# Kernel optimization log

Measured on AMD Instinct MI355X. Metric: run time of the kernel, lower is better.

## Reference

```python
import jax, jax.numpy as jnp
import numpy as np

B, C, D = 2, 2048, 1024   # batch, seq_len, hidden_size
I = 2048                  # intermediate_size (GLU hidden)
E, K = 8, 2               # n_experts, top_k
CF = 1.25                 # capacity factor


def setup_inputs() -> dict:
    key = jax.random.key(0)
    k1, k2, k3, k4 = jax.random.split(key, 4)
    scale = 0.02
    return {
        "hidden_states": jax.random.normal(k1, (B, C, D), jnp.float32),
        "Wg": jax.random.normal(k2, (E, D), jnp.float32) * scale,      # router gate weight [E, d]
        "W1": jax.random.normal(k3, (E, D, 2 * I), jnp.float32) * scale,  # expert in-proj
        "W2": jax.random.normal(k4, (E, I, D), jnp.float32) * scale,      # expert out-proj
    }


def reference(hidden_states, Wg, W1, W2):
    Bx, Cx, d = hidden_states.shape
    N = Bx * Cx
    cap = int(N * K * CF / E)  # exp_capacity (static)
    x = hidden_states.reshape(N, d)

    # --- router (eval mode: no noise) ---
    logits = x @ Wg.T                          # [N, E]
    top_v, top_i = jax.lax.top_k(logits, K)    # [N, K]
    gates = jax.nn.softmax(top_v, axis=-1)     # [N, K]

    # --- greedy capacity-limited assignment (token-major, then k), vectorized ---
    flat_e = top_i.reshape(N * K)              # expert id per (token, k) slot, in loop order
    gates_f = gates.reshape(N * K)
    tok = jnp.repeat(jnp.arange(N), K)         # token id per slot
    onehot = jax.nn.one_hot(flat_e, E, dtype=jnp.int32)
    pos = jnp.cumsum(onehot, axis=0) - 1       # running count per expert
    pos_f = jnp.take_along_axis(pos, flat_e[:, None], axis=1)[:, 0]
    keep = pos_f < cap                         # slots beyond capacity are dropped
    pos_safe = jnp.where(keep, pos_f, cap)     # out-of-range -> dropped by mode='drop'

    # --- dispatch: exp_batches[e, pos] = x[token] ---
    exp_batches = jnp.zeros((E, cap, d), x.dtype).at[flat_e, pos_safe].set(x[tok], mode='drop')

    # --- per-expert GLU MLP (batched over experts) ---
    h = jnp.einsum('ecd,edf->ecf', exp_batches, W1)       # [E, cap, 2I]
    inp, gate = jnp.split(h, 2, axis=-1)
    h = jax.nn.gelu(inp, approximate=False) * gate        # exact gelu, matches torch
    exp_out = jnp.einsum('eci,eid->ecd', h, W2)           # [E, cap, d]

    # --- combine: equals exp_mask.view(N,-1) @ exp_out.view(-1,d) ---
    gathered = exp_out[flat_e, jnp.minimum(pos_safe, cap - 1)]  # [N*K, d]
    contrib = jnp.where(keep, gates_f, 0.0)[:, None] * gathered
    out = jax.ops.segment_sum(contrib, tok, num_segments=N)    # [N, d]
    return out.reshape(Bx, Cx, d)
```

## Files before the change

### kernel.cpp

```cpp
#include <hip/hip_runtime.h>
#include <hip/hip_bf16.h>
#include <math.h>

#define N_TOK 4096
#define DIM   1024
#define NEXP  8
#define IDIM  2048
#define TWOI  4096
#define CAP   1280

#define W1_BLOCKS (64 * 16 * NEXP)
#define W2_BLOCKS (16 * 32 * NEXP)
#define ROUTER_BLOCKS (N_TOK / 4)

#define G1X 32
#define G1Y 10
#define G1_TRANS_Z ((W2_BLOCKS + G1X * G1Y - 1) / (G1X * G1Y))

using short8  = __attribute__((ext_vector_type(8))) short;
using floatx4 = __attribute__((ext_vector_type(4))) float;

__device__ __forceinline__ unsigned short f2b(float f) {
  __hip_bfloat16 h = __float2bfloat16(f);
  return *reinterpret_cast<unsigned short*>(&h);
}

__device__ __forceinline__ void async16(const unsigned short* g, unsigned short* l) {
  __builtin_amdgcn_global_load_lds(
      (const __attribute__((address_space(1))) unsigned int*)g,
      (__attribute__((address_space(3))) unsigned int*)l,
      16, 0, 0);
}

__global__ __launch_bounds__(256) void prologue_kernel(const float* __restrict__ W1,
                                                       unsigned short* __restrict__ w1t,
                                                       const float* __restrict__ x,
                                                       const float* __restrict__ Wg,
                                                       unsigned short* __restrict__ xb,
                                                       int* __restrict__ top_i,
                                                       float* __restrict__ gates) {
  __shared__ __align__(16) float smem_f[NEXP * DIM];
  int bid = blockIdx.x;
  int tid = threadIdx.x;

  if (bid < W1_BLOCKS) {
    float (*tile)[65] = reinterpret_cast<float (*)[65]>(smem_f);
    int e = bid >> 10;
    int t = bid & 1023;
    const int R = DIM, C = TWOI;
    int r0 = (t & 15) * 64;
    int c0 = (t >> 4) * 64;
    const float* s = W1 + (size_t)e * R * C;
    unsigned short* d = w1t + (size_t)e * R * C;
    int tr = tid >> 4, tc = (tid & 15) * 4;
#pragma unroll
    for (int i = 0; i < 4; i++) {
      float4 v = *reinterpret_cast<const float4*>(&s[(size_t)(r0 + tr + i * 16) * C + c0 + tc]);
      tile[tr + i * 16][tc]     = v.x;
      tile[tr + i * 16][tc + 1] = v.y;
      tile[tr + i * 16][tc + 2] = v.z;
      tile[tr + i * 16][tc + 3] = v.w;
    }
    __syncthreads();
#pragma unroll
    for (int j = 0; j < 4; j++) {
      int c = (tid >> 4) + j * 16;
      int r4 = (tid & 15) * 4;
      ushort4 o;
      o.x = f2b(tile[r4][c]);
      o.y = f2b(tile[r4 + 1][c]);
      o.z = f2b(tile[r4 + 2][c]);
      o.w = f2b(tile[r4 + 3][c]);
      *reinterpret_cast<ushort4*>(&d[(size_t)(c0 + c) * R + r0 + r4]) = o;
    }
  } else {
    int rb = bid - W1_BLOCKS;
    float* wg = smem_f;
    for (int i = tid * 4; i < NEXP * DIM; i += 256 * 4) {
      *reinterpret_cast<float4*>(wg + i) = *reinterpret_cast<const float4*>(Wg + i);
    }
    __syncthreads();
    int wave = tid >> 6, lane = tid & 63;
    int t = rb * 4 + wave;
    const float* xr = x + (size_t)t * DIM;
    unsigned short* xbr = xb + (size_t)t * DIM;
    double acc[NEXP];
#pragma unroll
    for (int e = 0; e < NEXP; e++) acc[e] = 0.0;
    for (int i = lane; i < DIM; i += 64) {
      float xf = xr[i];
      xbr[i] = f2b(xf);
      double xv = (double)xf;
#pragma unroll
      for (int e = 0; e < NEXP; e++) acc[e] += xv * (double)wg[e * DIM + i];
    }
#pragma unroll
    for (int e = 0; e < NEXP; e++) {
#pragma unroll
      for (int m = 1; m < 64; m <<= 1) acc[e] += __shfl_xor(acc[e], m, 64);
    }
    if (lane == 0) {
      int i0 = 0; double v0 = acc[0];
      for (int e = 1; e < NEXP; e++) { if (acc[e] > v0) { v0 = acc[e]; i0 = e; } }
      int i1 = -1; double v1 = -1e300;
      for (int e = 0; e < NEXP; e++) { if (e != i0 && acc[e] > v1) { v1 = acc[e]; i1 = e; } }
      double e1 = exp(v1 - v0);
      float g0 = (float)(1.0 / (1.0 + e1));
      float g1 = (float)(e1 / (1.0 + e1));
      top_i[t * 2] = i0; top_i[t * 2 + 1] = i1;
      gates[t * 2] = g0; gates[t * 2 + 1] = g1;
    }
  }
}

__global__ __launch_bounds__(1024) void scan_kernel(const int* __restrict__ top_i,
                                                    const float* __restrict__ gates,
                                                    int* __restrict__ rowtok,
                                                    int* __restrict__ rowslot,
                                                    float* __restrict__ rowgate,
                                                    float* __restrict__ tokgate,
                                                    int* __restrict__ cnt) {
  __shared__ int hist[NEXP][1024];
  int t = threadIdx.x;
  int s0 = t * 8;
  int eloc[8];
  int c[NEXP];
#pragma unroll
  for (int e = 0; e < NEXP; e++) c[e] = 0;
#pragma unroll
  for (int j = 0; j < 8; j++) { int e = top_i[s0 + j]; eloc[j] = e; c[e]++; }
#pragma unroll
  for (int e = 0; e < NEXP; e++) hist[e][t] = c[e];
  __syncthreads();
  for (int step = 1; step < 1024; step <<= 1) {
    int tmp[NEXP];
#pragma unroll
    for (int e = 0; e < NEXP; e++) tmp[e] = (t >= step) ? hist[e][t - step] : 0;
    __syncthreads();
#pragma unroll
    for (int e = 0; e < NEXP; e++) hist[e][t] += tmp[e];
    __syncthreads();
  }
  int base[NEXP];
#pragma unroll
  for (int e = 0; e < NEXP; e++) base[e] = hist[e][t] - c[e];
  if (t < NEXP) {
    int tot = hist[t][1023];
    cnt[t] = tot < CAP ? tot : CAP;
  }
#pragma unroll
  for (int j = 0; j < 8; j++) {
    int s = s0 + j;
    int e = eloc[j];
    int pos = base[e]++;
    bool keep = pos < CAP;
    tokgate[s] = keep ? gates[s] : 0.0f;
    if (keep) {
      rowtok[e * CAP + pos]  = s >> 1;
      rowslot[e * CAP + pos] = s & 1;
      rowgate[e * CAP + pos] = gates[s];
    }
  }
}

__global__ __launch_bounds__(256, 4) void gemm1_kernel(const unsigned short* __restrict__ xb,
                                                       const unsigned short* __restrict__ w1t,
                                                       const int* __restrict__ rowtok,
                                                       const int* __restrict__ cnt,
                                                       unsigned short* __restrict__ H,
                                                       const float* __restrict__ W2,
                                                       unsigned short* __restrict__ w2t) {
  __shared__ __align__(16) unsigned char smem[32768];
  int tid  = threadIdx.x;
  int z = blockIdx.z;

  if (z >= NEXP) {
    int id = (z - NEXP) * (G1X * G1Y) + blockIdx.y * G1X + blockIdx.x;
    if (id >= W2_BLOCKS) return;
    float (*tile)[65] = reinterpret_cast<float (*)[65]>(smem);
    int e = id >> 9;
    int t = id & 511;
    const int R = IDIM, C = DIM;
    int r0 = (t & 31) * 64;
    int c0 = (t >> 5) * 64;
    const float* s = W2 + (size_t)e * R * C;
    unsigned short* d = w2t + (size_t)e * R * C;
    int tr = tid >> 4, tc = (tid & 15) * 4;
#pragma unroll
    for (int i = 0; i < 4; i++) {
      float4 v = *reinterpret_cast<const float4*>(&s[(size_t)(r0 + tr + i * 16) * C + c0 + tc]);
      tile[tr + i * 16][tc]     = v.x;
      tile[tr + i * 16][tc + 1] = v.y;
      tile[tr + i * 16][tc + 2] = v.z;
      tile[tr + i * 16][tc + 3] = v.w;
    }
    __syncthreads();
#pragma unroll
    for (int j = 0; j < 4; j++) {
      int c = (tid >> 4) + j * 16;
      int r4 = (tid & 15) * 4;
      ushort4 o;
      o.x = f2b(tile[r4][c]);
      o.y = f2b(tile[r4 + 1][c]);
      o.z = f2b(tile[r4 + 2][c]);
      o.w = f2b(tile[r4 + 3][c]);
      *reinterpret_cast<ushort4*>(&d[(size_t)(c0 + c) * R + r0 + r4]) = o;
    }
    return;
  }

  int e  = z;
  int lin = blockIdx.y * G1X + blockIdx.x;
  int swz = (lin & 7) * (G1X * G1Y / 8) + (lin >> 3);
  int m0 = (swz / G1X) * 128;
  int i0 = (swz % G1X) * 64;
  int cnte = cnt[e];
  if (m0 >= cnte) return;

  unsigned short* As[2] = { (unsigned short*)smem,           (unsigned short*)(smem + 8192) };
  unsigned short* Bi[2] = { (unsigned short*)(smem + 16384), (unsigned short*)(smem + 20480) };
  unsigned short* Bg[2] = { (unsigned short*)(smem + 24576), (unsigned short*)(smem + 28672) };

  int lane = tid & 63;
  int wave = tid >> 6;

  int srA0 = wave * 32 + (lane >> 2);
  int srA1 = srA0 + 16;
  int srB  = wave * 16 + (lane >> 2);
  int sk   = (lane & 3) * 8;

  int ma0 = m0 + srA0, ma1 = m0 + srA1;
  int tok0 = (ma0 < cnte) ? rowtok[e * CAP + ma0] : 0;
  int tok1 = (ma1 < cnte) ? rowtok[e * CAP + ma1] : 0;

  const unsigned short* w1e = w1t + (size_t)e * TWOI * DIM;
  const unsigned short* gA0 = xb + (size_t)tok0 * DIM + sk;
  const unsigned short* gA1 = xb + (size_t)tok1 * DIM + sk;
  const unsigned short* gBi = w1e + (size_t)(i0 + srB) * DIM + sk;
  const unsigned short* gBg = w1e + (size_t)(i0 + srB + IDIM) * DIM + sk;

  int lane16 = lane & 15;
  int quad   = lane >> 4;
  int wm = (wave & 1) * 64;
  int wn = (wave >> 1) * 32;

  floatx4 acc_i[4][2], acc_g[4][2];
#pragma unroll
  for (int i = 0; i < 4; i++)
#pragma unroll
    for (int j = 0; j < 2; j++) {
      acc_i[i][j] = (floatx4){0.f, 0.f, 0.f, 0.f};
      acc_g[i][j] = (floatx4){0.f, 0.f, 0.f, 0.f};
    }

  for (int k0 = 0; k0 < DIM; k0 += 64) {
    __syncthreads();
#pragma unroll
    for (int b = 0; b < 2; b++) {
      int kk = k0 + b * 32;
      async16(gA0 + kk, As[b] + (wave * 2 + 0) * 512);
      async16(gA1 + kk, As[b] + (wave * 2 + 1) * 512);
      async16(gBi + kk, Bi[b] + wave * 512);
      async16(gBg + kk, Bg[b] + wave * 512);
    }
    __syncthreads();

#pragma unroll
    for (int b = 0; b < 2; b++) {
      short8 a[4];
#pragma unroll
      for (int i = 0; i < 4; i++)
        a[i] = *(const short8*)&As[b][(wm + i * 16 + lane16) * 32 + quad * 8];
#pragma unroll
      for (int j = 0; j < 2; j++) {
        short8 bi = *(const short8*)&Bi[b][(wn + j * 16 + lane16) * 32 + quad * 8];
#pragma unroll
        for (int i = 0; i < 4; i++)
          acc_i[i][j] = __builtin_amdgcn_mfma_f32_16x16x32_bf16(a[i], bi, acc_i[i][j], 0, 0, 0);
        short8 bg = *(const short8*)&Bg[b][(wn + j * 16 + lane16) * 32 + quad * 8];
#pragma unroll
        for (int i = 0; i < 4; i++)
          acc_g[i][j] = __builtin_amdgcn_mfma_f32_16x16x32_bf16(a[i], bg, acc_g[i][j], 0, 0, 0);
      }
    }
  }

  unsigned short* He = H + (size_t)e * CAP * IDIM;
#pragma unroll
  for (int i = 0; i < 4; i++) {
#pragma unroll
    for (int r = 0; r < 4; r++) {
      int m = m0 + wm + i * 16 + quad * 4 + r;
#pragma unroll
      for (int j = 0; j < 2; j++) {
        int n = i0 + wn + j * 16 + lane16;
        float vi = acc_i[i][j][r];
        float vg = acc_g[i][j][r];
        float h = 0.5f * vi * (1.0f + erff(vi * 0.70710678118654752f)) * vg;
        He[(size_t)m * IDIM + n] = f2b(h);
      }
    }
  }
}

__global__ __launch_bounds__(256, 4) void gemm2_kernel(const unsigned short* __restrict__ H,
                                                       const unsigned short* __restrict__ w2t,
                                                       const int* __restrict__ cnt,
                                                       const int* __restrict__ rowtok,
                                                       const int* __restrict__ rowslot,
                                                       const float* __restrict__ rowgate,
                                                       float* __restrict__ out2) {
  int e  = blockIdx.z;
  int lin = blockIdx.y * 8 + blockIdx.x;
  int swz = (lin & 7) * 10 + (lin >> 3);
  int m0 = (swz / 8) * 128;
  int n0 = (swz % 8) * 128;
  int cnte = cnt[e];
  if (m0 >= cnte) return;

  __shared__ __align__(16) unsigned char smem[32768];
  unsigned short* As[2] = { (unsigned short*)smem,           (unsigned short*)(smem + 8192) };
  unsigned short* Bs[2] = { (unsigned short*)(smem + 16384), (unsigned short*)(smem + 24576) };

  int tid  = threadIdx.x;
  int lane = tid & 63;
  int wave = tid >> 6;

  int sr0 = wave * 32 + (lane >> 2);
  int sr1 = sr0 + 16;
  int sk  = (lane & 3) * 8;

  const unsigned short* He  = H + (size_t)e * CAP * IDIM;
  const unsigned short* w2e = w2t + (size_t)e * DIM * IDIM;
  const unsigned short* gA0 = He + (size_t)(m0 + sr0) * IDIM + sk;
  const unsigned short* gA1 = He + (size_t)(m0 + sr1) * IDIM + sk;
  const unsigned short* gB0 = w2e + (size_t)(n0 + sr0) * IDIM + sk;
  const unsigned short* gB1 = w2e + (size_t)(n0 + sr1) * IDIM + sk;

  int lane16 = lane & 15;
  int quad   = lane >> 4;
  int wm = (wave & 1) * 64;
  int wn = (wave >> 1) * 64;

  floatx4 acc[4][4];
#pragma unroll
  for (int i = 0; i < 4; i++)
#pragma unroll
    for (int j = 0; j < 4; j++) acc[i][j] = (floatx4){0.f, 0.f, 0.f, 0.f};

  for (int k0 = 0; k0 < IDIM; k0 += 64) {
    __syncthreads();
#pragma unroll
    for (int b = 0; b < 2; b++) {
      int kk = k0 + b * 32;
      async16(gA0 + kk, As[b] + (wave * 2 + 0) * 512);
      async16(gA1 + kk, As[b] + (wave * 2 + 1) * 512);
      async16(gB0 + kk, Bs[b] + (wave * 2 + 0) * 512);
      async16(gB1 + kk, Bs[b] + (wave * 2 + 1) * 512);
    }
    __syncthreads();

#pragma unroll
    for (int b = 0; b < 2; b++) {
      short8 a[4];
#pragma unroll
      for (int i = 0; i < 4; i++)
        a[i] = *(const short8*)&As[b][(wm + i * 16 + lane16) * 32 + quad * 8];
#pragma unroll
      for (int j = 0; j < 4; j++) {
        short8 bb = *(const short8*)&Bs[b][(wn + j * 16 + lane16) * 32 + quad * 8];
#pragma unroll
        for (int i = 0; i < 4; i++)
          acc[i][j] = __builtin_amdgcn_mfma_f32_16x16x32_bf16(a[i], bb, acc[i][j], 0, 0, 0);
      }
    }
  }

#pragma unroll
  for (int i = 0; i < 4; i++) {
#pragma unroll
    for (int r = 0; r < 4; r++) {
      int m = m0 + wm + i * 16 + quad * 4 + r;
      if (m < cnte) {
        int tok = rowtok[e * CAP + m];
        int sl  = rowslot[e * CAP + m];
        float g = rowgate[e * CAP + m];
        float* orow = out2 + ((size_t)tok * 2 + sl) * DIM;
#pragma unroll
        for (int j = 0; j < 4; j++) {
          int n = n0 + wn + j * 16 + lane16;
          orow[n] = g * acc[i][j][r];
        }
      }
    }
  }
}

__global__ __launch_bounds__(256) void combine_kernel(const float* __restrict__ tokgate,
                                                      const float* __restrict__ out2,
                                                      float* __restrict__ out) {
  int t = blockIdx.x;
  int tid = threadIdx.x;
  float g0 = tokgate[t * 2], g1 = tokgate[t * 2 + 1];
  const float4* r0 = reinterpret_cast<const float4*>(out2 + (size_t)(t * 2) * DIM);
  const float4* r1 = reinterpret_cast<const float4*>(out2 + (size_t)(t * 2 + 1) * DIM);
  float4 a = r0[tid], b = r1[tid];
  float4 o;
  o.x = (g0 != 0.0f ? a.x : 0.0f) + (g1 != 0.0f ? b.x : 0.0f);
  o.y = (g0 != 0.0f ? a.y : 0.0f) + (g1 != 0.0f ? b.y : 0.0f);
  o.z = (g0 != 0.0f ? a.z : 0.0f) + (g1 != 0.0f ? b.z : 0.0f);
  o.w = (g0 != 0.0f ? a.w : 0.0f) + (g1 != 0.0f ? b.w : 0.0f);
  reinterpret_cast<float4*>(out + (size_t)t * DIM)[tid] = o;
}

extern "C" void kernel_launch(void* const* d_in, const int* in_sizes, int n_in,
                              void* d_out, int out_size, void* d_ws, size_t ws_size,
                              hipStream_t stream) {
  const float* x  = (const float*)d_in[0];
  const float* Wg = (const float*)d_in[1];
  const float* W1 = (const float*)d_in[2];
  const float* W2 = (const float*)d_in[3];
  float* out = (float*)d_out;

  char* ws = (char*)d_ws;
  size_t off = 0;
  auto alloc = [&](size_t bytes) -> void* {
    void* p = ws + off;
    off = (off + bytes + 255) & ~(size_t)255;
    return p;
  };
  int*   top_i   = (int*)alloc((size_t)N_TOK * 2 * sizeof(int));
  float* gates   = (float*)alloc((size_t)N_TOK * 2 * sizeof(float));
  int*   rowtok  = (int*)alloc((size_t)NEXP * CAP * sizeof(int));
  int*   rowslot = (int*)alloc((size_t)NEXP * CAP * sizeof(int));
  float* rowgate = (float*)alloc((size_t)NEXP * CAP * sizeof(float));
  float* tokgate = (float*)alloc((size_t)N_TOK * 2 * sizeof(float));
  int*   cnt     = (int*)alloc((size_t)NEXP * sizeof(int));
  unsigned short* xb  = (unsigned short*)alloc((size_t)N_TOK * DIM * 2);
  unsigned short* w1t = (unsigned short*)alloc((size_t)NEXP * TWOI * DIM * 2);
  unsigned short* w2t = (unsigned short*)alloc((size_t)NEXP * DIM * IDIM * 2);
  unsigned short* Hb  = (unsigned short*)alloc((size_t)NEXP * CAP * IDIM * 2);
  float* out2 = (float*)alloc((size_t)N_TOK * 2 * DIM * sizeof(float));
  if (off > ws_size) return;

  hipLaunchKernelGGL(prologue_kernel, dim3(W1_BLOCKS + ROUTER_BLOCKS), dim3(256), 0, stream,
                     W1, w1t, x, Wg, xb, top_i, gates);
  hipLaunchKernelGGL(scan_kernel, dim3(1), dim3(1024), 0, stream,
                     top_i, gates, rowtok, rowslot, rowgate, tokgate, cnt);
  hipLaunchKernelGGL(gemm1_kernel, dim3(G1X, G1Y, NEXP + G1_TRANS_Z), dim3(256), 0, stream,
                     xb, w1t, rowtok, cnt, Hb, W2, w2t);
  hipLaunchKernelGGL(gemm2_kernel, dim3(DIM / 128, CAP / 128, NEXP), dim3(256), 0, stream,
                     Hb, w2t, cnt, rowtok, rowslot, rowgate, out2);
  hipLaunchKernelGGL(combine_kernel, dim3(N_TOK), dim3(256), 0, stream,
                     tokgate, out2, out);
}
```

Baseline: 467.0 us.

## Fuse combine into gemm2 via atomic adds and drop tile swizzle

Removes the separate combine kernel and the out2 scratch buffer. The output is now zeroed in the router blocks of the prologue, and gemm2 atomically adds gate-weighted rows straight into it. This saves a launch and a round trip of the out2 buffer through memory. The block-index swizzle in both GEMMs is also removed in favour of plain row-major tile mapping. The trade-offs are scattered fp32 atomics, floating-point summation order that now varies between runs, and possibly worse cache locality from the unswizzled grid.

```diff
diff --git a/kernel.cpp b/kernel.cpp
--- a/kernel.cpp
+++ b/kernel.cpp
@@ -38,7 +38,8 @@
                                                        const float* __restrict__ Wg,
                                                        unsigned short* __restrict__ xb,
                                                        int* __restrict__ top_i,
-                                                       float* __restrict__ gates) {
+                                                       float* __restrict__ gates,
+                                                       float* __restrict__ out) {
   __shared__ __align__(16) float smem_f[NEXP * DIM];
   int bid = blockIdx.x;
   int tid = threadIdx.x;
@@ -75,6 +76,12 @@
     }
   } else {
     int rb = bid - W1_BLOCKS;
+    {
+      float4 z4 = {0.f, 0.f, 0.f, 0.f};
+      float4* ob = reinterpret_cast<float4*>(out + (size_t)rb * 4 * DIM);
+#pragma unroll
+      for (int i = 0; i < 4; i++) ob[tid + i * 256] = z4;
+    }
     float* wg = smem_f;
     for (int i = tid * 4; i < NEXP * DIM; i += 256 * 4) {
       *reinterpret_cast<float4*>(wg + i) = *reinterpret_cast<const float4*>(Wg + i);
@@ -116,9 +123,7 @@
 __global__ __launch_bounds__(1024) void scan_kernel(const int* __restrict__ top_i,
                                                     const float* __restrict__ gates,
                                                     int* __restrict__ rowtok,
-                                                    int* __restrict__ rowslot,
                                                     float* __restrict__ rowgate,
-                                                    float* __restrict__ tokgate,
                                                     int* __restrict__ cnt) {
   __shared__ int hist[NEXP][1024];
   int t = threadIdx.x;
@@ -153,11 +158,8 @@
     int s = s0 + j;
     int e = eloc[j];
     int pos = base[e]++;
-    bool keep = pos < CAP;
-    tokgate[s] = keep ? gates[s] : 0.0f;
-    if (keep) {
+    if (pos < CAP) {
       rowtok[e * CAP + pos]  = s >> 1;
-      rowslot[e * CAP + pos] = s & 1;
       rowgate[e * CAP + pos] = gates[s];
     }
   }
@@ -210,10 +212,8 @@
   }
 
   int e  = z;
-  int lin = blockIdx.y * G1X + blockIdx.x;
-  int swz = (lin & 7) * (G1X * G1Y / 8) + (lin >> 3);
-  int m0 = (swz / G1X) * 128;
-  int i0 = (swz % G1X) * 64;
+  int m0 = blockIdx.y * 128;
+  int i0 = blockIdx.x * 64;
   int cnte = cnt[e];
   if (m0 >= cnte) return;
 
@@ -307,14 +307,11 @@
                                                        const unsigned short* __restrict__ w2t,
                                                        const int* __restrict__ cnt,
                                                        const int* __restrict__ rowtok,
-                                                       const int* __restrict__ rowslot,
                                                        const float* __restrict__ rowgate,
-                                                       float* __restrict__ out2) {
+                                                       float* __restrict__ out) {
   int e  = blockIdx.z;
-  int lin = blockIdx.y * 8 + blockIdx.x;
-  int swz = (lin & 7) * 10 + (lin >> 3);
-  int m0 = (swz / 8) * 128;
-  int n0 = (swz % 8) * 128;
+  int m0 = blockIdx.y * 128;
+  int n0 = blockIdx.x * 128;
   int cnte = cnt[e];
   if (m0 >= cnte) return;
 
@@ -383,34 +380,16 @@
       int m = m0 + wm + i * 16 + quad * 4 + r;
       if (m < cnte) {
         int tok = rowtok[e * CAP + m];
-        int sl  = rowslot[e * CAP + m];
         float g = rowgate[e * CAP + m];
-        float* orow = out2 + ((size_t)tok * 2 + sl) * DIM;
+        float* orow = out + (size_t)tok * DIM;
 #pragma unroll
         for (int j = 0; j < 4; j++) {
           int n = n0 + wn + j * 16 + lane16;
-          orow[n] = g * acc[i][j][r];
+          atomicAdd(&orow[n], g * acc[i][j][r]);
         }
       }
     }
   }
-}
-
-__global__ __launch_bounds__(256) void combine_kernel(const float* __restrict__ tokgate,
-                                                      const float* __restrict__ out2,
-                                                      float* __restrict__ out) {
-  int t = blockIdx.x;
-  int tid = threadIdx.x;
-  float g0 = tokgate[t * 2], g1 = tokgate[t * 2 + 1];
-  const float4* r0 = reinterpret_cast<const float4*>(out2 + (size_t)(t * 2) * DIM);
-  const float4* r1 = reinterpret_cast<const float4*>(out2 + (size_t)(t * 2 + 1) * DIM);
-  float4 a = r0[tid], b = r1[tid];
-  float4 o;
-  o.x = (g0 != 0.0f ? a.x : 0.0f) + (g1 != 0.0f ? b.x : 0.0f);
-  o.y = (g0 != 0.0f ? a.y : 0.0f) + (g1 != 0.0f ? b.y : 0.0f);
-  o.z = (g0 != 0.0f ? a.z : 0.0f) + (g1 != 0.0f ? b.z : 0.0f);
-  o.w = (g0 != 0.0f ? a.w : 0.0f) + (g1 != 0.0f ? b.w : 0.0f);
-  reinterpret_cast<float4*>(out + (size_t)t * DIM)[tid] = o;
 }
 
 extern "C" void kernel_launch(void* const* d_in, const int* in_sizes, int n_in,
@@ -432,25 +411,20 @@
   int*   top_i   = (int*)alloc((size_t)N_TOK * 2 * sizeof(int));
   float* gates   = (float*)alloc((size_t)N_TOK * 2 * sizeof(float));
   int*   rowtok  = (int*)alloc((size_t)NEXP * CAP * sizeof(int));
-  int*   rowslot = (int*)alloc((size_t)NEXP * CAP * sizeof(int));
   float* rowgate = (float*)alloc((size_t)NEXP * CAP * sizeof(float));
-  float* tokgate = (float*)alloc((size_t)N_TOK * 2 * sizeof(float));
   int*   cnt     = (int*)alloc((size_t)NEXP * sizeof(int));
   unsigned short* xb  = (unsigned short*)alloc((size_t)N_TOK * DIM * 2);
   unsigned short* w1t = (unsigned short*)alloc((size_t)NEXP * TWOI * DIM * 2);
   unsigned short* w2t = (unsigned short*)alloc((size_t)NEXP * DIM * IDIM * 2);
   unsigned short* Hb  = (unsigned short*)alloc((size_t)NEXP * CAP * IDIM * 2);
-  float* out2 = (float*)alloc((size_t)N_TOK * 2 * DIM * sizeof(float));
   if (off > ws_size) return;
 
   hipLaunchKernelGGL(prologue_kernel, dim3(W1_BLOCKS + ROUTER_BLOCKS), dim3(256), 0, stream,
-                     W1, w1t, x, Wg, xb, top_i, gates);
+                     W1, w1t, x, Wg, xb, top_i, gates, out);
   hipLaunchKernelGGL(scan_kernel, dim3(1), dim3(1024), 0, stream,
-                     top_i, gates, rowtok, rowslot, rowgate, tokgate, cnt);
+                     top_i, gates, rowtok, rowgate, cnt);
   hipLaunchKernelGGL(gemm1_kernel, dim3(G1X, G1Y, NEXP + G1_TRANS_Z), dim3(256), 0, stream,
                      xb, w1t, rowtok, cnt, Hb, W2, w2t);
   hipLaunchKernelGGL(gemm2_kernel, dim3(DIM / 128, CAP / 128, NEXP), dim3(256), 0, stream,
-                     Hb, w2t, cnt, rowtok, rowslot, rowgate, out2);
-  hipLaunchKernelGGL(combine_kernel, dim3(N_TOK), dim3(256), 0, stream,
-                     tokgate, out2, out);
-}
+                     Hb, w2t, cnt, rowtok, rowgate, out);
+}
```

Result: faster. 438.5 us (-6.1%).
